# Performance work log

Hardware: AMD Instinct MI355X
Metric: run time of the kernel (lower is better)

## Reference

```python
import jax, jax.numpy as jnp
import numpy as np
import math

IN_F = 4096
OUT_F = 4096
NUM_FREQ = 16
RANK = 2
N_TOK = 8192


def setup_inputs() -> dict:
    key = jax.random.key(0)
    ks = jax.random.split(key, 10)
    x = jax.random.normal(ks[0], (N_TOK, IN_F), dtype=jnp.float32)
    amp = jax.random.normal(ks[1], (NUM_FREQ,), dtype=jnp.float32) * 0.1
    rf = jax.random.normal(ks[2], (NUM_FREQ,), dtype=jnp.float32) * 2.0
    cf = jax.random.normal(ks[3], (NUM_FREQ,), dtype=jnp.float32) * 2.0
    rp = jax.random.normal(ks[4], (NUM_FREQ,), dtype=jnp.float32) * 0.5
    cp = jax.random.normal(ks[5], (NUM_FREQ,), dtype=jnp.float32) * 0.5
    lora_A = jax.random.normal(ks[6], (OUT_F, RANK), dtype=jnp.float32) * 0.01
    lora_B = jax.random.normal(ks[7], (RANK, IN_F), dtype=jnp.float32) * 0.01
    alpha = jnp.float32(0.5)
    beta = jnp.float32(0.5)
    bias = jnp.zeros((OUT_F,), dtype=jnp.float32)
    return {"x": x, "amp": amp, "rf": rf, "cf": cf, "rp": rp, "cp": cp,
            "lora_A": lora_A, "lora_B": lora_B, "alpha": alpha, "beta": beta,
            "bias": bias}


def reference(x, amp, rf, cf, rp, cp, lora_A, lora_B, alpha, beta, bias):
    out_f, in_f = lora_A.shape[0], lora_B.shape[1]
    two_pi = 2.0 * math.pi
    r = jnp.linspace(0.0, two_pi, out_f, dtype=jnp.float32)  # [out_f]
    c = jnp.linspace(0.0, two_pi, in_f, dtype=jnp.float32)   # [in_f]
    # Fourier weight synthesis: sum_k amp[k] * outer(sin(r*rf[k]+rp[k]), cos(c*cf[k]+cp[k]))
    S = jnp.sin(r[None, :] * rf[:, None] + rp[:, None])  # [nf, out_f]
    C = jnp.cos(c[None, :] * cf[:, None] + cp[:, None])  # [nf, in_f]
    W_fourier = jnp.einsum('k,ko,ki->oi', amp, S, C)     # [out_f, in_f]
    W_lora = lora_A @ lora_B                              # [out_f, in_f]
    std = math.sqrt(2.0 / (in_f + out_f))
    a = jax.nn.sigmoid(alpha)
    b = jax.nn.sigmoid(beta)
    W = a * jnp.tanh(W_fourier) * std + b * jnp.tanh(W_lora) * std
    return x @ W.T + bias
```

## Files before the change

### kernel.cpp

```cpp
#include <hip/hip_runtime.h>
#include <hip/hip_bf16.h>
#include <cstdint>

typedef __attribute__((ext_vector_type(4))) float f32x4;
typedef __attribute__((ext_vector_type(4))) int i32x4;

#define IN_F 4096
#define OUT_F 4096
#define N_TOK 8192
#define NUM_FREQ 16
#define RROWS 4


__device__ inline float fast_tanh(float x) {
    float ax = fabsf(x);
    float e = __expf(2.0f * ax);
    float t = 1.0f - 2.0f / (e + 1.0f);
    return copysignf(t, x);
}

__device__ inline void load_lds16(const void* g, void* l) {
    __builtin_amdgcn_global_load_lds(
        (const __attribute__((address_space(1))) void*)(uintptr_t)g,
        (__attribute__((address_space(3))) void*)(uint32_t)(uintptr_t)l,
        16, 0, 0);
}

__device__ inline int q8(float v, float s) {
    int q = (int)rintf(v * s);
    return min(127, max(-127, q));
}

__device__ inline unsigned int pack4(int q0, int q1, int q2, int q3) {
    return (q0 & 255) | ((q1 & 255) << 8) | ((q2 & 255) << 16) |
           ((q3 & 255) << 24);
}

__global__ __launch_bounds__(256)
void prep(const float* __restrict__ x, signed char* __restrict__ xq,
          float* __restrict__ sx, const float* __restrict__ amp,
          const float* __restrict__ rf, const float* __restrict__ cf,
          const float* __restrict__ rp, const float* __restrict__ cp,
          const float* __restrict__ lA, const float* __restrict__ lB,
          const float* __restrict__ alpha, const float* __restrict__ beta,
          signed char* __restrict__ wq, float* __restrict__ sw) {
    const int tid = threadIdx.x;
    const int wave = tid >> 6;
    const int lane = tid & 63;
    __shared__ float s_s[RROWS][NUM_FREQ];
    __shared__ float red[RROWS][4];

    if (blockIdx.x < OUT_F / RROWS) {
        const int o0 = blockIdx.x * RROWS;
        const float step = 6.28318530717958647692f / 4095.0f;
        if (tid < RROWS * NUM_FREQ) {
            const int r = tid >> 4;
            const int k = tid & 15;
            s_s[r][k] =
                amp[k] * __sinf(step * (float)(o0 + r) * rf[k] + rp[k]);
        }
        __syncthreads();

        const int g = lane >> 2;
        const int q = lane & 3;

        float cfr[4], cpr[4];
#pragma unroll
        for (int e = 0; e < 4; ++e) {
            cfr[e] = cf[q * 4 + e];
            cpr[e] = cp[q * 4 + e];
        }
        float skr[RROWS][4];
#pragma unroll
        for (int r = 0; r < RROWS; ++r)
#pragma unroll
            for (int e = 0; e < 4; ++e) skr[r][e] = s_s[r][q * 4 + e];

        const float sa = 1.0f / (1.0f + __expf(-alpha[0]));
        const float sb = 1.0f / (1.0f + __expf(-beta[0]));
        const float stdv = 0.015625f;
        float a0r[RROWS], a1r[RROWS];
#pragma unroll
        for (int r = 0; r < RROWS; ++r) {
            a0r[r] = lA[(o0 + r) * 2 + 0];
            a1r[r] = lA[(o0 + r) * 2 + 1];
        }

        const int ibw = wave * 1024;
        float w[RROWS][16];

#pragma unroll
        for (int j = 0; j < 16; ++j) {
#pragma unroll
            for (int sq = 0; sq < 4; ++sq) {
                const int i = ibw + (j * 4 + sq) * 16 + g;
                const float ci = step * (float)i;
                float cv[4];
#pragma unroll
                for (int e = 0; e < 4; ++e)
                    cv[e] = __cosf(ci * cfr[e] + cpr[e]);
#pragma unroll
                for (int r = 0; r < RROWS; ++r) {
                    float p = skr[r][0] * cv[0] + skr[r][1] * cv[1] +
                              skr[r][2] * cv[2] + skr[r][3] * cv[3];
                    p += __shfl_xor(p, 1);
                    p += __shfl_xor(p, 2);
                    if (q == sq) w[r][j] = p;
                }
            }
        }

#pragma unroll
        for (int j = 0; j < 16; ++j) {
            const int i = ibw + (j * 4 + q) * 16 + g;
            const float b0 = lB[i];
            const float b1 = lB[IN_F + i];
#pragma unroll
            for (int r = 0; r < RROWS; ++r) {
                const float wl = a0r[r] * b0 + a1r[r] * b1;
                w[r][j] = sa * stdv * fast_tanh(w[r][j]) +
                          sb * stdv * fast_tanh(wl);
            }
        }

        float m[RROWS];
#pragma unroll
        for (int r = 0; r < RROWS; ++r) {
            float mm = 0.0f;
#pragma unroll
            for (int j = 0; j < 16; ++j) mm = fmaxf(mm, fabsf(w[r][j]));
#pragma unroll
            for (int off = 32; off > 0; off >>= 1)
                mm = fmaxf(mm, __shfl_xor(mm, off));
            m[r] = mm;
        }
        if (lane == 0) {
#pragma unroll
            for (int r = 0; r < RROWS; ++r) red[r][wave] = m[r];
        }
        __syncthreads();
#pragma unroll
        for (int r = 0; r < RROWS; ++r) {
            float mm = fmaxf(fmaxf(red[r][0], red[r][1]),
                             fmaxf(red[r][2], red[r][3]));
            m[r] = fmaxf(mm, 1e-20f);
        }

#pragma unroll
        for (int r = 0; r < RROWS; ++r) {
            const float s = 127.0f / m[r];
            signed char* wrow = wq + (size_t)(o0 + r) * IN_F;
#pragma unroll
            for (int j = 0; j < 16; ++j) {
                const int i = ibw + (j * 4 + q) * 16 + g;
                wrow[i] = (signed char)q8(w[r][j], s);
            }
        }
        if (tid == 0) {
#pragma unroll
            for (int r = 0; r < RROWS; ++r) sw[o0 + r] = m[r] / 127.0f;
        }
    } else {
        const int t = blockIdx.x - OUT_F / RROWS;
        const f32x4* xr = (const f32x4*)(x + (size_t)t * IN_F);
        f32x4 v[4];
#pragma unroll
        for (int j = 0; j < 4; ++j) v[j] = xr[tid + 256 * j];
        float m = 0.0f;
#pragma unroll
        for (int j = 0; j < 4; ++j)
#pragma unroll
            for (int e = 0; e < 4; ++e) m = fmaxf(m, fabsf(v[j][e]));
#pragma unroll
        for (int off = 32; off > 0; off >>= 1)
            m = fmaxf(m, __shfl_xor(m, off));
        if (lane == 0) red[0][wave] = m;
        __syncthreads();
        m = fmaxf(fmaxf(red[0][0], red[0][1]), fmaxf(red[0][2], red[0][3]));
        m = fmaxf(m, 1e-20f);
        const float s = 127.0f / m;
        unsigned int* orow = (unsigned int*)(xq + (size_t)t * IN_F);
#pragma unroll
        for (int j = 0; j < 4; ++j)
            orow[tid + 256 * j] =
                pack4(q8(v[j][0], s), q8(v[j][1], s), q8(v[j][2], s),
                      q8(v[j][3], s));
        if (tid == 0) sx[t] = m / 127.0f;
    }
}

#define BM 256
#define BN 256
#define SUBK 64

__global__ __launch_bounds__(512, 2)
void gemm_i8(const signed char* __restrict__ A, const signed char* __restrict__ B,
             const float* __restrict__ sx, const float* __restrict__ sw,
             const float* __restrict__ bias, float* __restrict__ C,
             int M, int N, int K) {
    __shared__ signed char lds[131072];

    const int tid = threadIdx.x;
    const int wave = tid >> 6;
    const int lane = tid & 63;

    const int bm = blockIdx.y * BM;
    const int bn = blockIdx.x * BN;

    const int srow = lane >> 2;
    const int scol = (((lane & 3) ^ ((lane >> 3) & 3)) << 4);

    const signed char* gA = A + (size_t)(bm + wave * 16 + srow) * K + scol;
    const signed char* gB = B + (size_t)(bn + wave * 16 + srow) * K + scol;
    const size_t rowK = (size_t)128 * K;

    const int lm = lane & 15;
    const int quad = lane >> 4;
    const int kq = ((quad ^ ((lm >> 1) & 3)) << 4);

    const int wm = (wave & 1) * 128;
    const int wn = (wave >> 1) * 64;
    const int aoff = (wm + lm) * SUBK + kq;
    const int boff = (wn + lm) * SUBK + kq;

    const int NT = K >> 6;

    auto STAGE_H0 = [&](int slot, int tt) {
        load_lds16(gA + (size_t)tt * SUBK, &lds[(slot << 14) + wave * 1024]);
        load_lds16(gB + (size_t)tt * SUBK,
                   &lds[65536 + (slot << 14) + wave * 1024]);
    };
    auto STAGE_H1 = [&](int slot, int tt) {
        load_lds16(gA + rowK + (size_t)tt * SUBK,
                   &lds[(slot << 14) + wave * 1024 + 8192]);
        load_lds16(gB + rowK + (size_t)tt * SUBK,
                   &lds[65536 + (slot << 14) + wave * 1024 + 8192]);
    };

    i32x4 acc[8][4] = {};
    i32x4 afl[4], afh[4], bva[4], bvb[4];

#define SLICE(T, BVN)                                                       \
    {                                                                       \
        const int slot_ = (T) & 3;                                          \
        const signed char* pa_ = &lds[slot_ << 14];                         \
        const signed char* pb_ = &lds[65536 + (slot_ << 14)];               \
        _Pragma("unroll") for (int i = 0; i < 4; ++i)                       \
            afl[i] = *(const i32x4*)(pa_ + aoff + i * 1024);                \
        _Pragma("unroll") for (int i = 0; i < 4; ++i)                       \
            BVN[i] = *(const i32x4*)(pb_ + boff + i * 1024);                \
        if ((T) + 3 < NT) STAGE_H0(((T) + 3) & 3, (T) + 3);                 \
        __builtin_amdgcn_s_barrier();                                       \
        asm volatile("s_waitcnt lgkmcnt(0)" ::: "memory");                  \
        __builtin_amdgcn_sched_barrier(0);                                  \
        __builtin_amdgcn_s_setprio(1);                                      \
        _Pragma("unroll") for (int im = 0; im < 4; ++im)                    \
            _Pragma("unroll") for (int in = 0; in < 4; ++in)                \
                acc[im][in] = __builtin_amdgcn_mfma_i32_16x16x64_i8(        \
                    afl[im], BVN[in], acc[im][in], 0, 0, 0);                \
        __builtin_amdgcn_s_setprio(0);                                      \
        __builtin_amdgcn_s_barrier();                                       \
        _Pragma("unroll") for (int i = 0; i < 4; ++i)                       \
            afh[i] = *(const i32x4*)(pa_ + aoff + 4096 + i * 1024);         \
        if ((T) + 3 < NT) STAGE_H1(((T) + 3) & 3, (T) + 3);                 \
        if ((T) < NT - 3)                                                   \
            asm volatile("s_waitcnt vmcnt(8)" ::: "memory");                \
        else if ((T) == NT - 3)                                             \
            asm volatile("s_waitcnt vmcnt(4)" ::: "memory");                \
        else                                                                \
            asm volatile("s_waitcnt vmcnt(0)" ::: "memory");                \
        __builtin_amdgcn_s_barrier();                                       \
        asm volatile("s_waitcnt lgkmcnt(0)" ::: "memory");                  \
        __builtin_amdgcn_sched_barrier(0);                                  \
        __builtin_amdgcn_s_setprio(1);                                      \
        _Pragma("unroll") for (int im = 0; im < 4; ++im)                    \
            _Pragma("unroll") for (int in = 0; in < 4; ++in)                \
                acc[im + 4][in] = __builtin_amdgcn_mfma_i32_16x16x64_i8(    \
                    afh[im], BVN[in], acc[im + 4][in], 0, 0, 0);            \
        __builtin_amdgcn_s_setprio(0);                                      \
        __builtin_amdgcn_s_barrier();                                       \
    }

    STAGE_H0(0, 0); STAGE_H1(0, 0);
    STAGE_H0(1, 1); STAGE_H1(1, 1);
    STAGE_H0(2, 2); STAGE_H1(2, 2);
    asm volatile("s_waitcnt vmcnt(8)" ::: "memory");
    __builtin_amdgcn_s_barrier();

    for (int t = 0; t < NT; t += 2) {
        SLICE(t, bva);
        SLICE(t + 1, bvb);
    }
#undef SLICE

    float sxv[8][4];
#pragma unroll
    for (int im = 0; im < 8; ++im)
#pragma unroll
        for (int r = 0; r < 4; ++r)
            sxv[im][r] = sx[bm + wm + im * 16 + quad * 4 + r];

#pragma unroll
    for (int in = 0; in < 4; ++in) {
        const int cn = bn + wn + in * 16 + lm;
        const float bv_ = bias[cn];
        const float scw = sw[cn];
#pragma unroll
        for (int im = 0; im < 8; ++im) {
            const int rm = bm + wm + im * 16 + quad * 4;
#pragma unroll
            for (int r = 0; r < 4; ++r)
                C[(size_t)(rm + r) * N + cn] =
                    (float)acc[im][in][r] * (sxv[im][r] * scw) + bv_;
        }
    }
}

extern "C" void kernel_launch(void* const* d_in, const int* in_sizes, int n_in,
                              void* d_out, int out_size, void* d_ws,
                              size_t ws_size, hipStream_t stream) {
    const float* x = (const float*)d_in[0];
    const float* amp = (const float*)d_in[1];
    const float* rf = (const float*)d_in[2];
    const float* cf = (const float*)d_in[3];
    const float* rp = (const float*)d_in[4];
    const float* cp = (const float*)d_in[5];
    const float* lA = (const float*)d_in[6];
    const float* lB = (const float*)d_in[7];
    const float* alpha = (const float*)d_in[8];
    const float* beta = (const float*)d_in[9];
    const float* bias = (const float*)d_in[10];
    float* out = (float*)d_out;

    signed char* wq = (signed char*)d_ws;
    signed char* xq = wq + (size_t)OUT_F * IN_F;
    float* sw = (float*)(xq + (size_t)N_TOK * IN_F);
    float* sx = sw + OUT_F;

    prep<<<OUT_F / RROWS + N_TOK, 256, 0, stream>>>(
        x, xq, sx, amp, rf, cf, rp, cp, lA, lB, alpha, beta, wq, sw);
    gemm_i8<<<dim3(OUT_F / BN, N_TOK / BM), 512, 0, stream>>>(
        xq, wq, sx, sw, bias, out, N_TOK, OUT_F, IN_F);
}
```

Baseline: 428.0 us.

## Load A fragments directly from global into registers, stage only B in LDS

The int8 GEMM stops staging the A tile through LDS. Each wave now loads its A fragments straight from global memory into double-buffered registers (afA/afB), and only B stays on the 4-slot LDS ring. This halves LDS use and traffic and merges the two half-slices into one MFMA batch per K step with fewer barriers. In exchange, A rows are read without cross-wave sharing, which raises register pressure and global/L2 traffic, and the vmcnt bookkeeping becomes harder to get right.

```diff
diff --git a/kernel.cpp b/kernel.cpp
--- a/kernel.cpp
+++ b/kernel.cpp
@@ -198,7 +198,7 @@
              const float* __restrict__ sx, const float* __restrict__ sw,
              const float* __restrict__ bias, float* __restrict__ C,
              int M, int N, int K) {
-    __shared__ signed char lds[131072];
+    __shared__ signed char ldsB[65536];
 
     const int tid = threadIdx.x;
     const int wave = tid >> 6;
@@ -209,87 +209,75 @@
 
     const int srow = lane >> 2;
     const int scol = (((lane & 3) ^ ((lane >> 3) & 3)) << 4);
-
-    const signed char* gA = A + (size_t)(bm + wave * 16 + srow) * K + scol;
     const signed char* gB = B + (size_t)(bn + wave * 16 + srow) * K + scol;
-    const size_t rowK = (size_t)128 * K;
+    const size_t rowK128 = (size_t)128 * K;
+
+    auto SB = [&](int slot, int tt) {
+        signed char* lb = &ldsB[(slot << 14) + wave * 1024];
+        load_lds16(gB + (size_t)tt * SUBK, lb);
+        load_lds16(gB + rowK128 + (size_t)tt * SUBK, lb + 8192);
+    };
 
     const int lm = lane & 15;
     const int quad = lane >> 4;
     const int kq = ((quad ^ ((lm >> 1) & 3)) << 4);
-
     const int wm = (wave & 1) * 128;
     const int wn = (wave >> 1) * 64;
-    const int aoff = (wm + lm) * SUBK + kq;
     const int boff = (wn + lm) * SUBK + kq;
 
+    const signed char* gAr = A + (size_t)(bm + wm + lm) * K + quad * 16;
+
     const int NT = K >> 6;
 
-    auto STAGE_H0 = [&](int slot, int tt) {
-        load_lds16(gA + (size_t)tt * SUBK, &lds[(slot << 14) + wave * 1024]);
-        load_lds16(gB + (size_t)tt * SUBK,
-                   &lds[65536 + (slot << 14) + wave * 1024]);
-    };
-    auto STAGE_H1 = [&](int slot, int tt) {
-        load_lds16(gA + rowK + (size_t)tt * SUBK,
-                   &lds[(slot << 14) + wave * 1024 + 8192]);
-        load_lds16(gB + rowK + (size_t)tt * SUBK,
-                   &lds[65536 + (slot << 14) + wave * 1024 + 8192]);
-    };
-
     i32x4 acc[8][4] = {};
-    i32x4 afl[4], afh[4], bva[4], bvb[4];
-
-#define SLICE(T, BVN)                                                       \
+    i32x4 afA[8], afB[8], bv[4];
+
+    SB(0, 0);
+    SB(1, 1);
+    SB(2, 2);
+    __builtin_amdgcn_sched_barrier(0);
+#pragma unroll
+    for (int i = 0; i < 8; ++i)
+        afA[i] = *(const i32x4*)(gAr + (size_t)(i * 16) * IN_F);
+    __builtin_amdgcn_sched_barrier(0);
+
+#define SLICE(T, CUR, NXT)                                                  \
     {                                                                       \
-        const int slot_ = (T) & 3;                                          \
-        const signed char* pa_ = &lds[slot_ << 14];                         \
-        const signed char* pb_ = &lds[65536 + (slot_ << 14)];               \
+        if ((T) == 0)                                                       \
+            asm volatile("s_waitcnt vmcnt(12)" ::: "memory");               \
+        else if ((T) < NT - 2)                                              \
+            asm volatile("s_waitcnt vmcnt(20)" ::: "memory");               \
+        else if ((T) == NT - 2)                                             \
+            asm volatile("s_waitcnt vmcnt(18)" ::: "memory");               \
+        else                                                                \
+            asm volatile("s_waitcnt vmcnt(16)" ::: "memory");               \
+        __builtin_amdgcn_s_barrier();                                       \
+        __builtin_amdgcn_sched_barrier(0);                                  \
+        const signed char* pb_ = &ldsB[((T) & 3) << 14];                    \
         _Pragma("unroll") for (int i = 0; i < 4; ++i)                       \
-            afl[i] = *(const i32x4*)(pa_ + aoff + i * 1024);                \
-        _Pragma("unroll") for (int i = 0; i < 4; ++i)                       \
-            BVN[i] = *(const i32x4*)(pb_ + boff + i * 1024);                \
-        if ((T) + 3 < NT) STAGE_H0(((T) + 3) & 3, (T) + 3);                 \
-        __builtin_amdgcn_s_barrier();                                       \
+            bv[i] = *(const i32x4*)(pb_ + boff + i * 1024);                 \
+        __builtin_amdgcn_sched_barrier(0);                                  \
+        if ((T) + 1 < NT) {                                                 \
+            _Pragma("unroll") for (int i = 0; i < 8; ++i)                   \
+                NXT[i] = *(const i32x4*)(gAr + (size_t)(i * 16) * IN_F +    \
+                                         ((T) + 1) * SUBK);                 \
+        }                                                                   \
+        __builtin_amdgcn_sched_barrier(0);                                  \
+        if ((T) + 3 < NT) SB(((T) + 3) & 3, (T) + 3);                       \
+        __builtin_amdgcn_sched_barrier(0);                                  \
         asm volatile("s_waitcnt lgkmcnt(0)" ::: "memory");                  \
         __builtin_amdgcn_sched_barrier(0);                                  \
         __builtin_amdgcn_s_setprio(1);                                      \
-        _Pragma("unroll") for (int im = 0; im < 4; ++im)                    \
+        _Pragma("unroll") for (int im = 0; im < 8; ++im)                    \
             _Pragma("unroll") for (int in = 0; in < 4; ++in)                \
                 acc[im][in] = __builtin_amdgcn_mfma_i32_16x16x64_i8(        \
-                    afl[im], BVN[in], acc[im][in], 0, 0, 0);                \
+                    CUR[im], bv[in], acc[im][in], 0, 0, 0);                 \
         __builtin_amdgcn_s_setprio(0);                                      \
-        __builtin_amdgcn_s_barrier();                                       \
-        _Pragma("unroll") for (int i = 0; i < 4; ++i)                       \
-            afh[i] = *(const i32x4*)(pa_ + aoff + 4096 + i * 1024);         \
-        if ((T) + 3 < NT) STAGE_H1(((T) + 3) & 3, (T) + 3);                 \
-        if ((T) < NT - 3)                                                   \
-            asm volatile("s_waitcnt vmcnt(8)" ::: "memory");                \
-        else if ((T) == NT - 3)                                             \
-            asm volatile("s_waitcnt vmcnt(4)" ::: "memory");                \
-        else                                                                \
-            asm volatile("s_waitcnt vmcnt(0)" ::: "memory");                \
-        __builtin_amdgcn_s_barrier();                                       \
-        asm volatile("s_waitcnt lgkmcnt(0)" ::: "memory");                  \
-        __builtin_amdgcn_sched_barrier(0);                                  \
-        __builtin_amdgcn_s_setprio(1);                                      \
-        _Pragma("unroll") for (int im = 0; im < 4; ++im)                    \
-            _Pragma("unroll") for (int in = 0; in < 4; ++in)                \
-                acc[im + 4][in] = __builtin_amdgcn_mfma_i32_16x16x64_i8(    \
-                    afh[im], BVN[in], acc[im + 4][in], 0, 0, 0);            \
-        __builtin_amdgcn_s_setprio(0);                                      \
-        __builtin_amdgcn_s_barrier();                                       \
     }
 
-    STAGE_H0(0, 0); STAGE_H1(0, 0);
-    STAGE_H0(1, 1); STAGE_H1(1, 1);
-    STAGE_H0(2, 2); STAGE_H1(2, 2);
-    asm volatile("s_waitcnt vmcnt(8)" ::: "memory");
-    __builtin_amdgcn_s_barrier();
-
     for (int t = 0; t < NT; t += 2) {
-        SLICE(t, bva);
-        SLICE(t + 1, bvb);
+        SLICE(t, afA, afB);
+        SLICE(t + 1, afB, afA);
     }
 #undef SLICE
 
```

Result: slower. 579.4 us (+35.4%).
